# Kernel tuning notes

Measured on AMD Instinct MI355X. Metric: run time of the kernel, lower is better.

Reference implementation:

```python
import jax, jax.numpy as jnp
import numpy as np

N, E = 100000, 1600000
IN_C, HID, OUT_C, EDGE_D, GRAPH_D = 32, 32, 8, 16, 16

def _lin_w(key, fan_in, fan_out):
    return jax.random.normal(key, (fan_in, fan_out), dtype=jnp.float32) * (1.0 / np.sqrt(fan_in))

def setup_inputs() -> dict:
    key = jax.random.key(0)
    ks = jax.random.split(key, 12)
    return {
        "x": jax.random.uniform(ks[0], (N, IN_C), dtype=jnp.float32),
        "edge_attr": jax.random.uniform(ks[1], (E, EDGE_D), dtype=jnp.float32),
        "graph_attr": jax.random.uniform(ks[2], (1, GRAPH_D), dtype=jnp.float32),
        "edge_index": jax.random.randint(ks[3], (2, E), 0, N, dtype=jnp.int32),
        "batch": jnp.zeros((N,), dtype=jnp.int32),
        "W_node": _lin_w(ks[4], IN_C, HID),
        "b_node": jnp.zeros((HID,), jnp.float32),
        "W_graph": _lin_w(ks[5], GRAPH_D, GRAPH_D),
        "b_graph": jnp.zeros((GRAPH_D,), jnp.float32),
        "W_edge_agg": _lin_w(ks[6], 2 * HID + EDGE_D + GRAPH_D, EDGE_D),
        "b_edge_agg": jnp.zeros((EDGE_D,), jnp.float32),
        "W_node_agg": _lin_w(ks[7], EDGE_D + HID + GRAPH_D, HID),
        "b_node_agg": jnp.zeros((HID,), jnp.float32),
        "W_sage_l": _lin_w(ks[8], HID, OUT_C),
        "b_sage_l": jnp.zeros((OUT_C,), jnp.float32),
        "W_sage_r": _lin_w(ks[9], HID, OUT_C),
    }

def _seg_mean(vals, idx, num_segments):
    # scatter-mean: sum per segment / count (count clamped to 1 for empty segments)
    sums = jax.ops.segment_sum(vals, idx, num_segments=num_segments)
    cnt = jax.ops.segment_sum(jnp.ones((vals.shape[0],), vals.dtype), idx, num_segments=num_segments)
    return sums / jnp.maximum(cnt, 1.0)[:, None]

def reference(x, edge_attr, graph_attr, edge_index, batch,
              W_node, b_node, W_graph, b_graph,
              W_edge_agg, b_edge_agg, W_node_agg, b_node_agg,
              W_sage_l, b_sage_l, W_sage_r):
    n = x.shape[0]
    row, col = edge_index[0], edge_index[1]
    # node / graph embeddings (plain linear, no activation)
    h_i = x @ W_node + b_node                       # [N, HID]
    h_G = graph_attr @ W_graph + b_graph            # [1, GRAPH_D]
    h_G_e = jnp.broadcast_to(h_G, (row.shape[0], h_G.shape[1]))
    # edge aggregator: gather both endpoints, concat, linear, relu
    edge_in = jnp.concatenate([h_i[row], h_i[col], edge_attr, h_G_e], axis=-1)  # [E, 96]
    h_edge_agg = jax.nn.relu(edge_in @ W_edge_agg + b_edge_agg)                 # [E, EDGE_D]
    # per-node mean of edges whose source == node (replaces O(N*E) python loop)
    m_N = _seg_mean(h_edge_agg, row, n)             # [N, EDGE_D]
    # node aggregator
    h_G_n = jnp.broadcast_to(h_G, (n, h_G.shape[1]))
    h_i2 = jax.nn.relu(jnp.concatenate([h_i, m_N, h_G_n], axis=-1) @ W_node_agg + b_node_agg)
    # SAGEConv (mean aggr): out = lin_l(mean_{j->i} x_j) + lin_r(x_i)
    agg = _seg_mean(h_i2[row], col, n)
    h_nodes = agg @ W_sage_l + b_sage_l + h_i2 @ W_sage_r  # [N, OUT_C]
    # global mean pool over batch assignment (single graph here)
    pooled = _seg_mean(h_nodes, batch, 1)           # [1, OUT_C]
    return jax.nn.log_softmax(pooled, axis=1)
```

## Files before the change

kernel.cpp:

```cpp
#include <hip/hip_runtime.h>
#include <hip/hip_fp16.h>

#define HID 32
#define IN_C 32
#define EDGE_D 16
#define GRAPH_D 16
#define OUT_C 8
#define STRIDE 48

__global__ void __launch_bounds__(256)
k_node_emb(const float* __restrict__ x,
           const float* __restrict__ W,
           const float* __restrict__ b,
           const float* __restrict__ graph_attr,
           const float* __restrict__ W_graph,
           const float* __restrict__ b_graph,
           const float* __restrict__ W_edge_agg,
           const float* __restrict__ b_edge_agg,
           const float* __restrict__ W_node_agg,
           const float* __restrict__ b_node_agg,
           float* __restrict__ bias_edge,
           float* __restrict__ bias_node,
           __half* __restrict__ h, int n) {
    __shared__ float hG[GRAPH_D];
    int t = threadIdx.x;
    if (blockIdx.x == 0 && t < GRAPH_D) {
        float acc = b_graph[t];
        for (int d = 0; d < GRAPH_D; d++)
            acc += graph_attr[d] * W_graph[d * GRAPH_D + t];
        hG[t] = acc;
    }
    __syncthreads();
    if (blockIdx.x == 0) {
        if (t < EDGE_D) {
            float acc = b_edge_agg[t];
            for (int d = 0; d < GRAPH_D; d++)
                acc += hG[d] * W_edge_agg[(2 * HID + EDGE_D + d) * EDGE_D + t];
            bias_edge[t] = acc;
        }
        if (t < HID) {
            float acc = b_node_agg[t];
            for (int d = 0; d < GRAPH_D; d++)
                acc += hG[d] * W_node_agg[(HID + EDGE_D + d) * HID + t];
            bias_node[t] = acc;
        }
    }

    int i = blockIdx.x * blockDim.x + t;
    if (i >= n) return;
    float in[IN_C];
    const float4* xr = (const float4*)(x + (size_t)i * IN_C);
#pragma unroll
    for (int q = 0; q < IN_C / 4; q++) {
        float4 v = xr[q];
        in[4 * q + 0] = v.x; in[4 * q + 1] = v.y;
        in[4 * q + 2] = v.z; in[4 * q + 3] = v.w;
    }
    float acc[HID];
#pragma unroll
    for (int j = 0; j < HID; j++) acc[j] = b[j];
#pragma unroll
    for (int k = 0; k < IN_C; k++) {
        float a = in[k];
#pragma unroll
        for (int j = 0; j < HID; j++) acc[j] += a * W[k * HID + j];
    }
    float4 packed[4];
    __half2* ph = (__half2*)packed;
#pragma unroll
    for (int j = 0; j < 16; j++)
        ph[j] = __floats2half2_rn(acc[2 * j], acc[2 * j + 1]);
    float4* hr = (float4*)(h + (size_t)i * HID);
#pragma unroll
    for (int q = 0; q < 4; q++) hr[q] = packed[q];
}

__global__ void __launch_bounds__(256)
k_edge_place(const int* __restrict__ ei,
             const __half* __restrict__ hi,
             const float* __restrict__ ea,
             const float* __restrict__ We,
             const float* __restrict__ biasE,
             int* __restrict__ cur_row,
             int* __restrict__ cur_col,
             __half* __restrict__ he_bucket, int E) {
    int e = blockIdx.x * blockDim.x + threadIdx.x;
    if (e >= E) return;
    int r = ei[e];
    int c = ei[E + e];
    int pr = atomicAdd(cur_row + r, 1);
    atomicAdd(cur_col + c, 1);

    float in[80];
    {
        float4 t[4];
        const float4* hr4 = (const float4*)(hi + (size_t)r * HID);
#pragma unroll
        for (int q = 0; q < 4; q++) t[q] = hr4[q];
        const __half2* hp = (const __half2*)t;
#pragma unroll
        for (int j = 0; j < 16; j++) {
            float2 f = __half22float2(hp[j]);
            in[2 * j] = f.x; in[2 * j + 1] = f.y;
        }
    }
    {
        float4 t[4];
        const float4* hc4 = (const float4*)(hi + (size_t)c * HID);
#pragma unroll
        for (int q = 0; q < 4; q++) t[q] = hc4[q];
        const __half2* hp = (const __half2*)t;
#pragma unroll
        for (int j = 0; j < 16; j++) {
            float2 f = __half22float2(hp[j]);
            in[32 + 2 * j] = f.x; in[32 + 2 * j + 1] = f.y;
        }
    }
    {
        const float4* er = (const float4*)(ea + (size_t)e * EDGE_D);
#pragma unroll
        for (int q = 0; q < 4; q++) {
            float4 v = er[q];
            in[64 + 4 * q + 0] = v.x; in[64 + 4 * q + 1] = v.y;
            in[64 + 4 * q + 2] = v.z; in[64 + 4 * q + 3] = v.w;
        }
    }
    float acc[EDGE_D];
#pragma unroll
    for (int j = 0; j < EDGE_D; j++) acc[j] = biasE[j];
#pragma unroll
    for (int k = 0; k < 80; k++) {
        float a = in[k];
#pragma unroll
        for (int j = 0; j < EDGE_D; j++) acc[j] += a * We[k * EDGE_D + j];
    }

    if (pr < STRIDE) {
        float4 packed[2];
        __half2* ph = (__half2*)packed;
#pragma unroll
        for (int j = 0; j < 8; j++)
            ph[j] = __floats2half2_rn(fmaxf(acc[2 * j], 0.f),
                                      fmaxf(acc[2 * j + 1], 0.f));
        float4* dst = (float4*)(he_bucket + ((size_t)r * STRIDE + pr) * EDGE_D);
        dst[0] = packed[0];
        dst[1] = packed[1];
    }
}

__global__ void __launch_bounds__(256)
k_reduce(const __half* __restrict__ hi,
         const __half* __restrict__ he_bucket,
         const int* __restrict__ cur_row,
         const int* __restrict__ batch,
         const float* __restrict__ Wna,
         const float* __restrict__ Wsl,
         const float* __restrict__ Wsr,
         const float* __restrict__ biasN,
         __half* __restrict__ zout,
         float* __restrict__ pool,
         float* __restrict__ ncnt, int n) {
    __shared__ float ms_s[256][EDGE_D + 1];
    __shared__ float red[4][OUT_C + 1];
    __shared__ float redc[4];
    int tid = threadIdx.x;
    int g = tid >> 4;
    int l = tid & 15;
    int blockBase = blockIdx.x * 256;

#pragma unroll 1
    for (int iter = 0; iter < 16; iter++) {
        int node = blockBase + iter * 16 + g;
        float a16[EDGE_D];
#pragma unroll
        for (int j = 0; j < EDGE_D; j++) a16[j] = 0.f;
        float inv = 0.f;
        if (node < n) {
            int cnt = cur_row[node];
            int d = cnt < STRIDE ? cnt : STRIDE;
            inv = 1.0f / fmaxf((float)cnt, 1.0f);
            const __half* base = he_bucket + (size_t)node * STRIDE * EDGE_D;
            for (int t = l; t < d; t += 16) {
                const float4* rp = (const float4*)(base + t * EDGE_D);
                float4 lo = rp[0], hi4 = rp[1];
                const __half2* hp0 = (const __half2*)&lo;
                const __half2* hp1 = (const __half2*)&hi4;
#pragma unroll
                for (int j = 0; j < 4; j++) {
                    float2 f0 = __half22float2(hp0[j]);
                    float2 f1 = __half22float2(hp1[j]);
                    a16[2 * j]     += f0.x; a16[2 * j + 1] += f0.y;
                    a16[8 + 2 * j] += f1.x; a16[8 + 2 * j + 1] += f1.y;
                }
            }
        }
#pragma unroll
        for (int m = 8; m >= 1; m >>= 1) {
#pragma unroll
            for (int k = 0; k < m; k++) {
                float send = (l & m) ? a16[k] : a16[k + m];
                float recv = __shfl_xor(send, m, 16);
                float keep = (l & m) ? a16[k + m] : a16[k];
                a16[k] = keep + recv;
            }
        }
        ms_s[iter * 16 + g][l] = a16[0] * inv;
    }
    __syncthreads();

    int i = blockBase + tid;
    float rvv[OUT_C];
#pragma unroll
    for (int j = 0; j < OUT_C; j++) rvv[j] = 0.f;
    float cc = 0.f;

    if (i < n) {
        float ms[EDGE_D];
#pragma unroll
        for (int k = 0; k < EDGE_D; k++) ms[k] = ms_s[tid][k];

        float hr[HID];
        {
            float4 t[4];
            const float4* hrow = (const float4*)(hi + (size_t)i * HID);
#pragma unroll
            for (int q = 0; q < 4; q++) t[q] = hrow[q];
            const __half2* hp = (const __half2*)t;
#pragma unroll
            for (int j = 0; j < 16; j++) {
                float2 f = __half22float2(hp[j]);
                hr[2 * j] = f.x; hr[2 * j + 1] = f.y;
            }
        }
        float h2[HID];
#pragma unroll
        for (int j = 0; j < HID; j++) h2[j] = biasN[j];
#pragma unroll
        for (int k = 0; k < HID; k++) {
            float a = hr[k];
#pragma unroll
            for (int j = 0; j < HID; j++) h2[j] += a * Wna[k * HID + j];
        }
#pragma unroll
        for (int k = 0; k < EDGE_D; k++) {
            float a = ms[k];
#pragma unroll
            for (int j = 0; j < HID; j++) h2[j] += a * Wna[(HID + k) * HID + j];
        }
#pragma unroll
        for (int j = 0; j < HID; j++) h2[j] = fmaxf(h2[j], 0.f);

        float zv[OUT_C];
#pragma unroll
        for (int j = 0; j < OUT_C; j++) zv[j] = 0.f;
#pragma unroll
        for (int k = 0; k < HID; k++) {
            float a = h2[k];
#pragma unroll
            for (int j = 0; j < OUT_C; j++) {
                zv[j]  += a * Wsl[k * OUT_C + j];
                rvv[j] += a * Wsr[k * OUT_C + j];
            }
        }
        float4 packed;
        __half2* ph = (__half2*)&packed;
#pragma unroll
        for (int j = 0; j < 4; j++)
            ph[j] = __floats2half2_rn(zv[2 * j], zv[2 * j + 1]);
        *(float4*)(zout + (size_t)i * OUT_C) = packed;
        if (batch[i] == 0) cc = 1.f; else {
#pragma unroll
            for (int j = 0; j < OUT_C; j++) rvv[j] = 0.f;
        }
    }
#pragma unroll
    for (int off = 32; off > 0; off >>= 1) {
#pragma unroll
        for (int j = 0; j < OUT_C; j++) rvv[j] += __shfl_down(rvv[j], off, 64);
        cc += __shfl_down(cc, off, 64);
    }
    int w = tid >> 6;
    if ((tid & 63) == 0) {
#pragma unroll
        for (int j = 0; j < OUT_C; j++) red[w][j] = rvv[j];
        redc[w] = cc;
    }
    __syncthreads();
    if (tid < OUT_C) {
        float s = red[0][tid] + red[1][tid] + red[2][tid] + red[3][tid];
        atomicAdd(pool + tid, s);
    }
    if (tid == OUT_C) {
        atomicAdd(ncnt, redc[0] + redc[1] + redc[2] + redc[3]);
    }
}

__global__ void __launch_bounds__(256)
k_pool(const int* __restrict__ ei,
       const __half* __restrict__ z,
       const int* __restrict__ cur_col,
       float* __restrict__ pool, int E) {
    __shared__ float red[4][OUT_C + 1];
    int tid = threadIdx.x;
    int e = blockIdx.x * blockDim.x + tid;
    float w8[OUT_C];
#pragma unroll
    for (int j = 0; j < OUT_C; j++) w8[j] = 0.f;
    if (e < E) {
        int r = ei[e];
        int c = ei[E + e];
        float inv = 1.0f / fmaxf((float)cur_col[c], 1.0f);
        float4 t = *(const float4*)(z + (size_t)r * OUT_C);
        const __half2* hp = (const __half2*)&t;
#pragma unroll
        for (int j = 0; j < 4; j++) {
            float2 f = __half22float2(hp[j]);
            w8[2 * j]     = f.x * inv;
            w8[2 * j + 1] = f.y * inv;
        }
    }
#pragma unroll
    for (int off = 32; off > 0; off >>= 1) {
#pragma unroll
        for (int j = 0; j < OUT_C; j++) w8[j] += __shfl_down(w8[j], off, 64);
    }
    int w = tid >> 6;
    if ((tid & 63) == 0) {
#pragma unroll
        for (int j = 0; j < OUT_C; j++) red[w][j] = w8[j];
    }
    __syncthreads();
    if (tid < OUT_C) {
        float s = red[0][tid] + red[1][tid] + red[2][tid] + red[3][tid];
        atomicAdd(pool + tid, s);
    }
}

__global__ void k_final(const float* __restrict__ pool,
                        const float* __restrict__ ncnt,
                        const float* __restrict__ bsl,
                        float* __restrict__ out) {
    if (threadIdx.x == 0 && blockIdx.x == 0) {
        float c = fmaxf(ncnt[0], 1.0f);
        float p[OUT_C];
        float m = -1e30f;
#pragma unroll
        for (int j = 0; j < OUT_C; j++) {
            p[j] = pool[j] / c + bsl[j];
            m = fmaxf(m, p[j]);
        }
        float s = 0.f;
#pragma unroll
        for (int j = 0; j < OUT_C; j++) s += expf(p[j] - m);
        float l = logf(s);
#pragma unroll
        for (int j = 0; j < OUT_C; j++) out[j] = p[j] - m - l;
    }
}

extern "C" void kernel_launch(void* const* d_in, const int* in_sizes, int n_in,
                              void* d_out, int out_size, void* d_ws, size_t ws_size,
                              hipStream_t stream) {
    const float* x          = (const float*)d_in[0];
    const float* edge_attr  = (const float*)d_in[1];
    const float* graph_attr = (const float*)d_in[2];
    const int*   edge_index = (const int*)d_in[3];
    const int*   batch      = (const int*)d_in[4];
    const float* W_node     = (const float*)d_in[5];
    const float* b_node     = (const float*)d_in[6];
    const float* W_graph    = (const float*)d_in[7];
    const float* b_graph    = (const float*)d_in[8];
    const float* W_edge_agg = (const float*)d_in[9];
    const float* b_edge_agg = (const float*)d_in[10];
    const float* W_node_agg = (const float*)d_in[11];
    const float* b_node_agg = (const float*)d_in[12];
    const float* W_sage_l   = (const float*)d_in[13];
    const float* b_sage_l   = (const float*)d_in[14];
    const float* W_sage_r   = (const float*)d_in[15];

    const int n = in_sizes[0] / IN_C;
    const int E = in_sizes[3] / 2;

    char* wsb = (char*)d_ws;
    int*  cur_row = (int*)wsb;
    int*  cur_col = cur_row + n;
    float* pool   = (float*)(cur_col + n);
    float* ncnt   = pool + 8;
    size_t zero_bytes = ((size_t)2 * n + 16) * 4;
    size_t off = zero_bytes;
    __half* he_bucket = (__half*)(wsb + off); off += (size_t)n * STRIDE * EDGE_D * 2;
    __half* h_i  = (__half*)(wsb + off); off += (size_t)n * HID * 2;
    __half* zarr = (__half*)(wsb + off); off += (size_t)n * OUT_C * 2;
    float* biasE = (float*)(wsb + off);  off += 16 * 4;
    float* biasN = (float*)(wsb + off);

    hipMemsetAsync(wsb, 0, zero_bytes, stream);

    k_node_emb<<<(n + 255) / 256, 256, 0, stream>>>(x, W_node, b_node,
                                                    graph_attr, W_graph, b_graph,
                                                    W_edge_agg, b_edge_agg,
                                                    W_node_agg, b_node_agg,
                                                    biasE, biasN, h_i, n);

    k_edge_place<<<(E + 255) / 256, 256, 0, stream>>>(edge_index, h_i, edge_attr,
                                                      W_edge_agg, biasE,
                                                      cur_row, cur_col,
                                                      he_bucket, E);

    k_reduce<<<(n + 255) / 256, 256, 0, stream>>>(h_i, he_bucket, cur_row, batch,
                                                  W_node_agg, W_sage_l, W_sage_r,
                                                  biasN, zarr, pool, ncnt, n);

    k_pool<<<(E + 255) / 256, 256, 0, stream>>>(edge_index, zarr, cur_col, pool, E);

    k_final<<<1, 64, 0, stream>>>(pool, ncnt, b_sage_l, (float*)d_out);
}
```

Before: 573.9 us.

## Fold memset and final softmax into kernels; halve nodes per reduce block

Zeroing of the counters is moved from a separate memset into the node-embedding kernel. The final log-softmax kernel is removed and done by the last block of the pooling kernel, which it detects with an atomic done counter. The reduce kernel now handles 128 nodes per block instead of 256, preloading counts into shared memory, which doubles the block count for more parallelism on the bucket reduction. The trade-offs are extra fence and atomic traffic, and idle threads during the dense second phase of reduce.

Measured after the change: 708.9 us. 23.5% more time.

```diff
diff --git a/kernel.cpp b/kernel.cpp
--- a/kernel.cpp
+++ b/kernel.cpp
@@ -21,9 +21,14 @@
            const float* __restrict__ b_node_agg,
            float* __restrict__ bias_edge,
            float* __restrict__ bias_node,
+           int* __restrict__ zero_base, int zero_count,
            __half* __restrict__ h, int n) {
     __shared__ float hG[GRAPH_D];
     int t = threadIdx.x;
+    for (int idx = blockIdx.x * blockDim.x + t; idx < zero_count;
+         idx += gridDim.x * blockDim.x)
+        zero_base[idx] = 0;
+
     if (blockIdx.x == 0 && t < GRAPH_D) {
         float acc = b_graph[t];
         for (int d = 0; d < GRAPH_D; d++)
@@ -148,6 +153,7 @@
     }
 }
 
+#define RNODES 128
 __global__ void __launch_bounds__(256)
 k_reduce(const __half* __restrict__ hi,
          const __half* __restrict__ he_bucket,
@@ -160,38 +166,39 @@
          __half* __restrict__ zout,
          float* __restrict__ pool,
          float* __restrict__ ncnt, int n) {
-    __shared__ float ms_s[256][EDGE_D + 1];
+    __shared__ float ms_s[RNODES][EDGE_D + 1];
+    __shared__ int cnt_s[RNODES];
     __shared__ float red[4][OUT_C + 1];
     __shared__ float redc[4];
     int tid = threadIdx.x;
     int g = tid >> 4;
     int l = tid & 15;
-    int blockBase = blockIdx.x * 256;
-
-#pragma unroll 1
-    for (int iter = 0; iter < 16; iter++) {
-        int node = blockBase + iter * 16 + g;
+    int base = blockIdx.x * RNODES;
+
+    if (tid < RNODES)
+        cnt_s[tid] = (base + tid < n) ? cur_row[base + tid] : 0;
+    __syncthreads();
+
+    for (int iter = 0; iter < RNODES / 16; iter++) {
+        int node = base + iter * 16 + g;
+        int cnt = cnt_s[iter * 16 + g];
+        int d = cnt < STRIDE ? cnt : STRIDE;
+        float inv = 1.0f / fmaxf((float)cnt, 1.0f);
         float a16[EDGE_D];
 #pragma unroll
         for (int j = 0; j < EDGE_D; j++) a16[j] = 0.f;
-        float inv = 0.f;
-        if (node < n) {
-            int cnt = cur_row[node];
-            int d = cnt < STRIDE ? cnt : STRIDE;
-            inv = 1.0f / fmaxf((float)cnt, 1.0f);
-            const __half* base = he_bucket + (size_t)node * STRIDE * EDGE_D;
-            for (int t = l; t < d; t += 16) {
-                const float4* rp = (const float4*)(base + t * EDGE_D);
-                float4 lo = rp[0], hi4 = rp[1];
-                const __half2* hp0 = (const __half2*)&lo;
-                const __half2* hp1 = (const __half2*)&hi4;
-#pragma unroll
-                for (int j = 0; j < 4; j++) {
-                    float2 f0 = __half22float2(hp0[j]);
-                    float2 f1 = __half22float2(hp1[j]);
-                    a16[2 * j]     += f0.x; a16[2 * j + 1] += f0.y;
-                    a16[8 + 2 * j] += f1.x; a16[8 + 2 * j + 1] += f1.y;
-                }
+        const __half* bb = he_bucket + (size_t)node * STRIDE * EDGE_D;
+        for (int t = l; t < d; t += 16) {
+            const float4* rp = (const float4*)(bb + t * EDGE_D);
+            float4 lo = rp[0], hi4 = rp[1];
+            const __half2* hp0 = (const __half2*)&lo;
+            const __half2* hp1 = (const __half2*)&hi4;
+#pragma unroll
+            for (int j = 0; j < 4; j++) {
+                float2 f0 = __half22float2(hp0[j]);
+                float2 f1 = __half22float2(hp1[j]);
+                a16[2 * j]     += f0.x; a16[2 * j + 1] += f0.y;
+                a16[8 + 2 * j] += f1.x; a16[8 + 2 * j + 1] += f1.y;
             }
         }
 #pragma unroll
@@ -208,13 +215,13 @@
     }
     __syncthreads();
 
-    int i = blockBase + tid;
+    int i = base + tid;
     float rvv[OUT_C];
 #pragma unroll
     for (int j = 0; j < OUT_C; j++) rvv[j] = 0.f;
     float cc = 0.f;
 
-    if (i < n) {
+    if (tid < RNODES && i < n) {
         float ms[EDGE_D];
 #pragma unroll
         for (int k = 0; k < EDGE_D; k++) ms[k] = ms_s[tid][k];
@@ -299,7 +306,11 @@
 k_pool(const int* __restrict__ ei,
        const __half* __restrict__ z,
        const int* __restrict__ cur_col,
-       float* __restrict__ pool, int E) {
+       float* __restrict__ pool,
+       const float* __restrict__ ncnt,
+       int* __restrict__ done,
+       const float* __restrict__ bsl,
+       float* __restrict__ out, int E) {
     __shared__ float red[4][OUT_C + 1];
     int tid = threadIdx.x;
     int e = blockIdx.x * blockDim.x + tid;
@@ -333,28 +344,31 @@
     if (tid < OUT_C) {
         float s = red[0][tid] + red[1][tid] + red[2][tid] + red[3][tid];
         atomicAdd(pool + tid, s);
-    }
-}
-
-__global__ void k_final(const float* __restrict__ pool,
-                        const float* __restrict__ ncnt,
-                        const float* __restrict__ bsl,
-                        float* __restrict__ out) {
-    if (threadIdx.x == 0 && blockIdx.x == 0) {
-        float c = fmaxf(ncnt[0], 1.0f);
-        float p[OUT_C];
-        float m = -1e30f;
-#pragma unroll
-        for (int j = 0; j < OUT_C; j++) {
-            p[j] = pool[j] / c + bsl[j];
-            m = fmaxf(m, p[j]);
-        }
-        float s = 0.f;
-#pragma unroll
-        for (int j = 0; j < OUT_C; j++) s += expf(p[j] - m);
-        float l = logf(s);
-#pragma unroll
-        for (int j = 0; j < OUT_C; j++) out[j] = p[j] - m - l;
+        __threadfence();
+    }
+    __syncthreads();
+    if (tid == 0) {
+        int old = __hip_atomic_fetch_add(done, 1, __ATOMIC_ACQ_REL,
+                                         __HIP_MEMORY_SCOPE_AGENT);
+        if (old == (int)gridDim.x - 1) {
+            float c = fmaxf(__hip_atomic_load(ncnt, __ATOMIC_RELAXED,
+                                              __HIP_MEMORY_SCOPE_AGENT), 1.0f);
+            float p[OUT_C];
+            float m = -1e30f;
+#pragma unroll
+            for (int j = 0; j < OUT_C; j++) {
+                float pj = __hip_atomic_load(pool + j, __ATOMIC_RELAXED,
+                                             __HIP_MEMORY_SCOPE_AGENT);
+                p[j] = pj / c + bsl[j];
+                m = fmaxf(m, p[j]);
+            }
+            float s = 0.f;
+#pragma unroll
+            for (int j = 0; j < OUT_C; j++) s += expf(p[j] - m);
+            float l = logf(s);
+#pragma unroll
+            for (int j = 0; j < OUT_C; j++) out[j] = p[j] - m - l;
+        }
     }
 }
 
@@ -386,32 +400,33 @@
     int*  cur_col = cur_row + n;
     float* pool   = (float*)(cur_col + n);
     float* ncnt   = pool + 8;
-    size_t zero_bytes = ((size_t)2 * n + 16) * 4;
-    size_t off = zero_bytes;
+    int*  done    = (int*)(ncnt + 1);
+    int   zero_count = 2 * n + 16;
+    size_t off = (size_t)zero_count * 4;
     __half* he_bucket = (__half*)(wsb + off); off += (size_t)n * STRIDE * EDGE_D * 2;
     __half* h_i  = (__half*)(wsb + off); off += (size_t)n * HID * 2;
     __half* zarr = (__half*)(wsb + off); off += (size_t)n * OUT_C * 2;
     float* biasE = (float*)(wsb + off);  off += 16 * 4;
     float* biasN = (float*)(wsb + off);
 
-    hipMemsetAsync(wsb, 0, zero_bytes, stream);
-
     k_node_emb<<<(n + 255) / 256, 256, 0, stream>>>(x, W_node, b_node,
                                                     graph_attr, W_graph, b_graph,
                                                     W_edge_agg, b_edge_agg,
                                                     W_node_agg, b_node_agg,
-                                                    biasE, biasN, h_i, n);
+                                                    biasE, biasN,
+                                                    cur_row, zero_count, h_i, n);
 
     k_edge_place<<<(E + 255) / 256, 256, 0, stream>>>(edge_index, h_i, edge_attr,
                                                       W_edge_agg, biasE,
                                                       cur_row, cur_col,
                                                       he_bucket, E);
 
-    k_reduce<<<(n + 255) / 256, 256, 0, stream>>>(h_i, he_bucket, cur_row, batch,
-                                                  W_node_agg, W_sage_l, W_sage_r,
-                                                  biasN, zarr, pool, ncnt, n);
-
-    k_pool<<<(E + 255) / 256, 256, 0, stream>>>(edge_index, zarr, cur_col, pool, E);
-
-    k_final<<<1, 64, 0, stream>>>(pool, ncnt, b_sage_l, (float*)d_out);
+    k_reduce<<<(n + RNODES - 1) / RNODES, 256, 0, stream>>>(h_i, he_bucket, cur_row,
+                                                            batch, W_node_agg,
+                                                            W_sage_l, W_sage_r,
+                                                            biasN, zarr, pool, ncnt, n);
+
+    k_pool<<<(E + 255) / 256, 256, 0, stream>>>(edge_index, zarr, cur_col,
+                                                pool, ncnt, done, b_sage_l,
+                                                (float*)d_out, E);
 }
```
